# Kernel optimization log

Measured on AMD Instinct MI355X. Metric: run time of the kernel, lower is better.

## Reference

```python
import jax, jax.numpy as jnp
import numpy as np

N_LAYER = 4
N_HEAD = 8
D_HEAD = 64
D_MODEL = 512
D_INNER = 2048
NMT = 16  # num_mem_tokens
BSZ = 1
QLEN = 2048


def _rel_shift(x):
    # x: [i, j, b, n] -> Transformer-XL relative shift
    i, j, b, n = x.shape
    zero_pad = jnp.zeros((i, 1, b, n), dtype=x.dtype)
    x_padded = jnp.concatenate([zero_pad, x], axis=1)  # [i, j+1, b, n]
    x_padded = x_padded.reshape(j + 1, i, b, n)
    return x_padded[1:].reshape(i, j, b, n)


def _layer_norm(x, g, b):
    mu = jnp.mean(x, axis=-1, keepdims=True)
    var = jnp.mean(jnp.square(x - mu), axis=-1, keepdims=True)
    return (x - mu) / jnp.sqrt(var + 1e-5) * g + b


def setup_inputs() -> dict:
    key = jax.random.key(0)
    ks = jax.random.split(key, 12)
    s = 0.02
    return {
        "word_emb": jax.random.normal(ks[0], (BSZ, QLEN, D_MODEL), jnp.float32),
        "mem_tokens": jax.random.normal(ks[1], (NMT, BSZ, D_MODEL), jnp.float32),
        "Wqkv": jax.random.normal(ks[2], (N_LAYER, D_MODEL, 3 * N_HEAD * D_HEAD), jnp.float32) * s,
        "Wr": jax.random.normal(ks[3], (N_LAYER, D_MODEL, N_HEAD * D_HEAD), jnp.float32) * s,
        "Wo": jax.random.normal(ks[4], (N_LAYER, N_HEAD * D_HEAD, D_MODEL), jnp.float32) * s,
        "ln1_scale": jnp.ones((N_LAYER, D_MODEL), jnp.float32),
        "ln1_bias": jnp.zeros((N_LAYER, D_MODEL), jnp.float32),
        "ffn_W1": jax.random.normal(ks[5], (N_LAYER, D_MODEL, D_INNER), jnp.float32) * s,
        "ffn_b1": jnp.zeros((N_LAYER, D_INNER), jnp.float32),
        "ffn_W2": jax.random.normal(ks[6], (N_LAYER, D_INNER, D_MODEL), jnp.float32) * s,
        "ffn_b2": jnp.zeros((N_LAYER, D_MODEL), jnp.float32),
        "ln2_scale": jnp.ones((N_LAYER, D_MODEL), jnp.float32),
        "ln2_bias": jnp.zeros((N_LAYER, D_MODEL), jnp.float32),
        "r_w_bias": jax.random.normal(ks[7], (N_HEAD, D_HEAD), jnp.float32) * s,
        "r_r_bias": jax.random.normal(ks[8], (N_HEAD, D_HEAD), jnp.float32) * s,
    }


def reference(word_emb, mem_tokens, Wqkv, Wr, Wo, ln1_scale, ln1_bias,
              ffn_W1, ffn_b1, ffn_W2, ffn_b2, ln2_scale, ln2_bias,
              r_w_bias, r_r_bias):
    # word_emb: [B, Q, D] -> [Q, B, D]; prepend + append mem tokens (mem_at_end)
    w = jnp.transpose(word_emb, (1, 0, 2))
    w = jnp.concatenate([mem_tokens, w, mem_tokens], axis=0)  # [T, B, D]
    T, B = w.shape[0], w.shape[1]

    # causal mask (mlen=0) with mem-token exceptions, True = masked
    mask = jnp.triu(jnp.ones((T, T), dtype=bool), k=1)
    mask = mask.at[:NMT, :NMT].set(False)          # read-mem block attends to itself
    mask = mask.at[-NMT:, -NMT:].set(False)        # write-mem block attends to itself

    # sinusoidal relative positional embedding, pos_seq = T-1 .. 0
    inv_freq = 1.0 / (10000.0 ** (jnp.arange(0, D_MODEL, 2, dtype=jnp.float32) / D_MODEL))
    pos_seq = jnp.arange(T - 1, -1, -1.0, dtype=jnp.float32)
    sinusoid = pos_seq[:, None] * inv_freq[None, :]
    pos_emb = jnp.concatenate([jnp.sin(sinusoid), jnp.cos(sinusoid)], axis=-1)  # [T, D]

    scale = 1.0 / np.sqrt(D_HEAD)
    for l in range(N_LAYER):
        heads = w @ Wqkv[l]                                        # [T, B, 3*H*Dh]
        q, k, v = jnp.split(heads, 3, axis=-1)
        q = q.reshape(T, B, N_HEAD, D_HEAD)
        k = k.reshape(T, B, N_HEAD, D_HEAD)
        v = v.reshape(T, B, N_HEAD, D_HEAD)
        r = (pos_emb @ Wr[l]).reshape(T, N_HEAD, D_HEAD)           # [T, H, Dh]

        AC = jnp.einsum('ibnd,jbnd->ijbn', q + r_w_bias, k)
        BD = _rel_shift(jnp.einsum('ibnd,jnd->ijbn', q + r_r_bias, r))
        score = (AC + BD) * scale                                  # [T, T, B, H]
        score = jnp.where(mask[:, :, None, None], -1e30, score)
        prob = jax.nn.softmax(score, axis=1)
        attn_vec = jnp.einsum('ijbn,jbnd->ibnd', prob, v).reshape(T, B, N_HEAD * D_HEAD)

        w = _layer_norm(w + attn_vec @ Wo[l], ln1_scale[l], ln1_bias[l])  # post-LN
        ff = jax.nn.relu(w @ ffn_W1[l] + ffn_b1[l]) @ ffn_W2[l] + ffn_b2[l]
        w = _layer_norm(w + ff, ln2_scale[l], ln2_bias[l])
    return w  # [T, B, D]
```

## Files before the change

### kernel.cpp

```cpp
#include <hip/hip_runtime.h>
#include <hip/hip_bf16.h>
#include <math.h>
#include <stdint.h>

#define TT 2080
#define DM 512
#define DI 2048
#define NH 8
#define DH 64
#define NMTOK 16
#define NLAYER 4
#define QKV_N 1536
#define ATT_SCALE 0.125f
#define SPLIT 8
#define WT_STRIDE 3407872
#define QRP_HEAD 2200640

typedef short bf16x8 __attribute__((ext_vector_type(8)));
typedef float f32x4 __attribute__((ext_vector_type(4)));
typedef unsigned short ushort_t;

__device__ __forceinline__ ushort_t f2bf(float f) {
  __hip_bfloat16 h = __float2bfloat16(f);
  return *reinterpret_cast<ushort_t*>(&h);
}
__device__ __forceinline__ float bfbits2f(unsigned int hi_bits) {
  return __uint_as_float(hi_bits);
}
__device__ __forceinline__ float bf2f(ushort_t u) {
  return bfbits2f(((unsigned int)u) << 16);
}
__device__ __forceinline__ void unpack8(uint4 v, float* f) {
  f[0] = bfbits2f(v.x << 16); f[1] = bfbits2f(v.x & 0xffff0000u);
  f[2] = bfbits2f(v.y << 16); f[3] = bfbits2f(v.y & 0xffff0000u);
  f[4] = bfbits2f(v.z << 16); f[5] = bfbits2f(v.z & 0xffff0000u);
  f[6] = bfbits2f(v.w << 16); f[7] = bfbits2f(v.w & 0xffff0000u);
}
__device__ __forceinline__ unsigned int pack2(ushort_t lo, ushort_t hi) {
  return (unsigned int)lo | ((unsigned int)hi << 16);
}
__device__ __forceinline__ void barrier_lds() {
  asm volatile("s_waitcnt lgkmcnt(0)" ::: "memory");
  __builtin_amdgcn_s_barrier();
}
__device__ __forceinline__ void barrier_all() {
  asm volatile("s_waitcnt vmcnt(0) lgkmcnt(0)" ::: "memory");
  __builtin_amdgcn_s_barrier();
}
__device__ __forceinline__ void gload16(const ushort_t* g, ushort_t* l) {
  __builtin_amdgcn_global_load_lds(
      (__attribute__((address_space(1))) void*)(uintptr_t)g,
      (__attribute__((address_space(3))) void*)(uintptr_t)l, 16, 0, 0);
}
__device__ __forceinline__ size_t qr_rowbase(int i) {
  int m = i & 3;
  int r = (m == 0) ? 0 : (m == 1) ? 3 : (m == 2) ? 5 : 6;
  return (size_t)i * (i + 33) / 2 + 6 * (i >> 2) + r;
}
__device__ __forceinline__ size_t ft512(int r, int c) {
  return (((size_t)(r >> 4) * 16 + (c >> 5)) << 9) + (((c >> 3) & 3) << 7) +
         ((r & 15) << 3) + (c & 7);
}

__global__ __launch_bounds__(256) void k_prep(
    const float* __restrict__ Wqkv, const float* __restrict__ Wr,
    const float* __restrict__ Wo, const float* __restrict__ W1,
    const float* __restrict__ W2, ushort_t* __restrict__ dstAll,
    const float* __restrict__ we, const float* __restrict__ mem,
    float* __restrict__ w, ushort_t* __restrict__ wbft,
    ushort_t* __restrict__ posft) {
  const int tid = threadIdx.x;
  if (blockIdx.x >= 13312) {
    int idx = (blockIdx.x - 13312) * 256 + tid;
    if (idx >= TT * DM) return;
    int t = idx >> 9, d = idx & 511;
    float v;
    if (t < NMTOK) v = mem[t * DM + d];
    else if (t < NMTOK + 2048) v = we[(t - NMTOK) * DM + d];
    else v = mem[(t - (NMTOK + 2048)) * DM + d];
    w[idx] = v;
    wbft[ft512(t, d)] = f2bf(v);
    float p = (float)(TT - 1 - t);
    int i2 = d & 255;
    float freq = __expf(-0.035977892f * (float)i2);
    float ang = p * freq;
    posft[ft512(t, d)] = f2bf((d < 256) ? __sinf(ang) : __cosf(ang));
    return;
  }
  __shared__ float tl[32][33];
  const int l = blockIdx.x / 3328;
// ... 165 lines not shown
  const int nIter = (kEnd - kBeg) >> 6;
  stage(smem, kt0);
  __syncthreads();
  for (int t = 0; t < nIter; t += 2) {
    if (t + 1 < nIter) stage(smem + 12288, kt0 + (t + 1) * 2);
    compute(smem);
    __syncthreads();
    if (t + 2 < nIter) stage(smem, kt0 + (t + 2) * 2);
    compute(smem + 12288);
    __syncthreads();
  }

#pragma unroll
  for (int i = 0; i < 2; ++i) {
    const int rowb = m0 + wm + i * 16 + quad * 4;
#pragma unroll
    for (int j = 0; j < 4; ++j) {
      const int col = n0 + wn + j * 16 + lm;
      const float bv = (flags & 1) ? bias[col] : 0.f;
#pragma unroll
      for (int t2 = 0; t2 < 4; ++t2) {
        const int row = rowb + t2;
        float v = acc[i][j][t2] + bv;
        if (flags & 2) v = fmaxf(v, 0.f);
        if (omode == 0) {
          Cf[(size_t)row * N + col] = v;
        } else if (omode == 1) {
          Cb[(size_t)row * N + col] = f2bf(v);
        } else if (omode == 2) {
          Cb[(((size_t)(row >> 4) * cftKT + (col >> 5)) << 9) +
             (((col >> 3) & 3) << 7) + ((row & 15) << 3) + (col & 7)] = f2bf(v);
        } else if (omode == 3) {
          Cb[ft512(row, col)] = f2bf(v + rwb[col]);
          aux[(size_t)row * DM + col] = f2bf(v + rrb[col]);
        } else if (omode == 4) {
          Cb[ft512(row, col - 512)] = f2bf(v);
        } else {
          const int dv = col - 1024;
          Cb[((size_t)(dv >> 4) * 65 + (row >> 5)) * 512 +
             (((row >> 3) & 3) << 7) + ((dv & 15) << 3) + (row & 7)] = f2bf(v);
        }
      }
    }
  }
}

__global__ __launch_bounds__(256) void k_gemm_qkvwr_ft(
    const ushort_t* __restrict__ wbft, const ushort_t* __restrict__ posft,
    const ushort_t* __restrict__ qkvT, const ushort_t* __restrict__ wrT,
    ushort_t* __restrict__ qwft, ushort_t* __restrict__ kft,
    ushort_t* __restrict__ vtft, ushort_t* __restrict__ rbg,
    ushort_t* __restrict__ qrb, const float* __restrict__ rwb,
    const float* __restrict__ rrb) {
  __shared__ ushort_t smem[24576];
  int m0 = blockIdx.y * 64;
  if (m0 + 64 > TT) m0 = TT - 64;
  const int bx = blockIdx.x;
  if (bx < 12) {
    const int om = (bx < 4) ? 3 : (bx < 8 ? 4 : 5);
    ushort_t* dst = (om == 3) ? qwft : (om == 4) ? kft : vtft;
    gemm_ft_body(smem, wbft, qkvT, nullptr, QKV_N, DM, 0, DM, m0, bx * 128,
                 0, om, nullptr, dst, 0, qrb, rwb, rrb);
  } else {
    gemm_ft_body(smem, posft, wrT, nullptr, DM, DM, 0, DM, m0, (bx - 12) * 128,
                 0, 1, nullptr, rbg, 0, nullptr, nullptr, nullptr);
  }
}

__global__ __launch_bounds__(256) void k_ffn1_ft(const ushort_t* __restrict__ wbft,
                                                 const ushort_t* __restrict__ w1T,
                                                 const float* __restrict__ b1l,
                                                 ushort_t* __restrict__ ff1ft) {
  __shared__ ushort_t smem[24576];
  int m0 = blockIdx.y * 64;
  if (m0 + 64 > TT) m0 = TT - 64;
  gemm_ft_body(smem, wbft, w1T, b1l, DI, DM, 0, DM, m0, blockIdx.x * 128,
               1 | 2, 2, nullptr, ff1ft, DI >> 5, nullptr, nullptr, nullptr);
}

__global__ __launch_bounds__(256) void k_ffn2_ft(const ushort_t* __restrict__ ff1ft,
                                                 const ushort_t* __restrict__ w2T,
                                                 const float* __restrict__ b2l,
                                                 float* __restrict__ ff2p) {
  __shared__ ushort_t smem[24576];
  int m0 = blockIdx.y * 64;
  if (m0 + 64 > TT) m0 = TT - 64;
  const int s = blockIdx.z;
  gemm_ft_body(smem, ff1ft, w2T, b2l, DM, DI, s * 512, s * 512 + 512, m0,
               blockIdx.x * 128, (s == 0) ? 1 : 0, 0,
               ff2p + (size_t)s * TT * DM, nullptr, 0, nullptr, nullptr, nullptr);
}

__global__ __launch_bounds__(256) void k_qr(const ushort_t* __restrict__ qrb,
                                            const ushort_t* __restrict__ rbg,
                                            ushort_t* __restrict__ qrp) {
  const int h = blockIdx.z;
  const int m0 = blockIdx.y * 32, n0 = blockIdx.x * 64;
  if (!(n0 == 0 || n0 + 63 >= TT - 32 - m0)) return;
  __shared__ short As[32][72];
  __shared__ short Bs[64][72];
  const int tid = threadIdx.x;
  const int lane = tid & 63, wv = tid >> 6;
  const int wm = (wv >> 1) * 16, wn = (wv & 1) * 32;
  const int lm = lane & 15, quad = lane >> 4;
  const int sr = tid >> 3, sc8 = (tid & 7) * 8;
  const uint4 zero4 = make_uint4(0, 0, 0, 0);

  *(uint4*)&As[sr][sc8] = *(const uint4*)&qrb[(size_t)(m0 + sr) * DM + h * DH + sc8];
  int br0 = n0 + sr, br1 = n0 + sr + 32;
  *(uint4*)&Bs[sr][sc8] =
      (br0 < TT) ? *(const uint4*)&rbg[(size_t)br0 * DM + h * DH + sc8] : zero4;
  *(uint4*)&Bs[sr + 32][sc8] =
      (br1 < TT) ? *(const uint4*)&rbg[(size_t)br1 * DM + h * DH + sc8] : zero4;
  __syncthreads();

  f32x4 acc[2];
  acc[0] = (f32x4)(0.f); acc[1] = (f32x4)(0.f);
#pragma unroll
  for (int kk = 0; kk < 64; kk += 32) {
    bf16x8 a = *(const bf16x8*)&As[wm + lm][kk + quad * 8];
    bf16x8 b0 = *(const bf16x8*)&Bs[wn + lm][kk + quad * 8];
    bf16x8 b1 = *(const bf16x8*)&Bs[wn + 16 + lm][kk + quad * 8];
    acc[0] = __builtin_amdgcn_mfma_f32_16x16x32_bf16(a, b0, acc[0], 0, 0, 0);
    acc[1] = __builtin_amdgcn_mfma_f32_16x16x32_bf16(a, b1, acc[1], 0, 0, 0);
  }
  const size_t hb = (size_t)h * QRP_HEAD;
#pragma unroll
  for (int nt = 0; nt < 2; ++nt) {
    int col = n0 + wn + nt * 16 + lm;
    if (col >= TT) continue;
#pragma unroll
    for (int t = 0; t < 4; ++t) {
      int row = m0 + wm + quad * 4 + t;
      float v = acc[nt][t];
      int p = row + col - (TT - 1);
      size_t rb = hb + qr_rowbase(row);
      if (p >= 0) qrp[rb + p] = f2bf(v);
      if (col < 16) qrp[rb + row + 1 + col] = f2bf(v);
    }
  }
}

__global__ __launch_bounds__(256) void k_attn(const ushort_t* __restrict__ qwft,
                                              const ushort_t* __restrict__ kft,
                                              const ushort_t* __restrict__ vtft,
                                              const ushort_t* __restrict__ qrp,
                                              float* __restrict__ mlP,
                                              ushort_t* __restrict__ opP) {
  const int h = blockIdx.y;
  const int qt = 64 - blockIdx.x;
  const int c = blockIdx.z;
  if (c > qt) return;
  const int i0 = qt * 32;
  const int tid = threadIdx.x;
  const int lane = tid & 63, wv = tid >> 6;
  const int lm = lane & 15, quad = lane >> 4;

  __shared__ ushort_t qwl[2048];
  __shared__ ushort_t kl[2][2048];
  __shared__ ushort_t vtl[2][2048];
  __shared__ ushort_t pbl[1024];
  __shared__ float st[32][34];
  __shared__ float m_s[32], l_s[32], alpha_s[32];

  const int ii = tid >> 3, g = tid & 7, jjb = g * 4;
  const int i = i0 + ii;
  const size_t hb = (size_t)h * QRP_HEAD;
  const size_t qrRow = hb + qr_rowbase(i);
  const size_t qrRowW = hb + qr_rowbase(i + 1) + i + 2;

  const int sblk = tid >> 6, sln = tid & 63;
  auto stageKV = [&](int j0, int buf) {
    gload16(kft + (((size_t)((j0 >> 4) + (sblk >> 1)) * 16) + h * 2 + (sblk & 1)) * 512 +
                (sln << 3),
            kl[buf] + (tid << 3));
    gload16(vtft + (((size_t)(h * 4 + sblk)) * 65 + (j0 >> 5)) * 512 + (sln << 3),
            vtl[buf] + (tid << 3));
  };

  gload16(qwft + (((size_t)((i0 >> 4) + (sblk >> 1)) * 16) + h * 2 + (sblk & 1)) * 512 +
              (sln << 3),
          qwl + (tid << 3));
  stageKV(c * 32, 0);
  if (tid < 32) { m_s[tid] = -INFINITY; l_s[tid] = 0.f; }
  barrier_all();

  const int acit = wv >> 1, acjt = wv & 1;
  bf16x8 aQ[2];
#pragma unroll
  for (int kt = 0; kt < 2; ++kt)
    aQ[kt] = *(const bf16x8*)&qwl[(acit * 2 + kt) * 512 + (lane << 3)];

  f32x4 oA = (f32x4)(0.f);
  f32x4 oB = (f32x4)(0.f);

  int cur = 0;
  for (int jt = c; jt <= qt; jt += SPLIT) {
    const int j0 = jt * 32;
    uint2 qr2 = *(const uint2*)&qrp[qrRow + j0 + jjb];
    if (jt + SPLIT <= qt) stageKV((jt + SPLIT) * 32, cur ^ 1);

    {
      f32x4 ac = (f32x4)(0.f);
#pragma unroll
      for (int kt = 0; kt < 2; ++kt) {
        bf16x8 b = *(const bf16x8*)&kl[cur][(acjt * 2 + kt) * 512 + (lane << 3)];
        ac = __builtin_amdgcn_mfma_f32_16x16x32_bf16(aQ[kt], b, ac, 0, 0, 0);
      }
#pragma unroll
      for (int t = 0; t < 4; ++t)
        st[acit * 16 + quad * 4 + t][acjt * 16 + lm] = ac[t];
    }
    barrier_lds();

    {
      float bd4[4];
      bd4[0] = bf2f((ushort_t)(qr2.x & 0xffffu));
      bd4[1] = bf2f((ushort_t)(qr2.x >> 16));
      bd4[2] = bf2f((ushort_t)(qr2.y & 0xffffu));
      bd4[3] = bf2f((ushort_t)(qr2.y >> 16));
      float sreg[4];
      if (jt < qt) {
#pragma unroll
        for (int u = 0; u < 4; ++u)
          sreg[u] = (st[ii][jjb + u] + bd4[u]) * ATT_SCALE;
      } else {
#pragma unroll
        for (int u = 0; u < 4; ++u) {
          int j = j0 + jjb + u;
          float acv = st[ii][jjb + u];
          float s;
          if (j <= i) {
            s = (acv + bd4[u]) * ATT_SCALE;
          } else {
            bool inmem = (i < NMTOK && j < NMTOK) ||
                         (i >= TT - NMTOK && j >= TT - NMTOK);
            if (!inmem) s = -1e30f;
            else if (j == i + 1) s = acv * ATT_SCALE;
            else s = (acv + bf2f(qrp[qrRowW + (j - i - 2)])) * ATT_SCALE;
          }
          sreg[u] = s;
        }
      }
      float tmax = fmaxf(fmaxf(sreg[0], sreg[1]), fmaxf(sreg[2], sreg[3]));
#pragma unroll
      for (int off = 1; off < 8; off <<= 1) tmax = fmaxf(tmax, __shfl_xor(tmax, off));
      const float mold = m_s[ii];
      const float mnew = fmaxf(mold, tmax);
      const float alpha = __expf(mold - mnew);
      float p[4], psum = 0.f;
#pragma unroll
      for (int u = 0; u < 4; ++u) { p[u] = __expf(sreg[u] - mnew); psum += p[u]; }
#pragma unroll
      for (int off = 1; off < 8; off <<= 1) psum += __shfl_xor(psum, off);
      uint2 pk;
      pk.x = pack2(f2bf(p[0]), f2bf(p[1]));
      pk.y = pack2(f2bf(p[2]), f2bf(p[3]));
      *(uint2*)&pbl[(size_t)(ii >> 4) * 512 + (g >> 1) * 128 + (ii & 15) * 8 +
                    (g & 1) * 4] = pk;
      if (g == 0) {
        m_s[ii] = mnew;
        l_s[ii] = l_s[ii] * alpha + psum;
        alpha_s[ii] = alpha;
      }
    }
    barrier_lds();

    {
      float a0 = alpha_s[lm], a1 = alpha_s[16 + lm];
      bf16x8 av = *(const bf16x8*)&vtl[cur][wv * 512 + (lane << 3)];
      bf16x8 p0 = *(const bf16x8*)&pbl[(lane << 3)];
      bf16x8 p1 = *(const bf16x8*)&pbl[512 + (lane << 3)];
#pragma unroll
      for (int t = 0; t < 4; ++t) { oA[t] *= a0; oB[t] *= a1; }
      oA = __builtin_amdgcn_mfma_f32_16x16x32_bf16(av, p0, oA, 0, 0, 0);
      oB = __builtin_amdgcn_mfma_f32_16x16x32_bf16(av, p1, oB, 0, 0, 0);
    }
    barrier_all();
    cur ^= 1;
  }

  {
    const int pidx = (qt * NH + h) * SPLIT + c;
    if (tid < 32) {
      mlP[(size_t)pidx * 64 + tid] = m_s[tid];
      mlP[(size_t)pidx * 64 + 32 + tid] = l_s[tid];
    }
    ushort_t o0[4], o1[4];
#pragma unroll
    for (int t = 0; t < 4; ++t) { o0[t] = f2bf(oA[t]); o1[t] = f2bf(oB[t]); }
    size_t ob = (size_t)pidx * 2048;
    *(uint2*)&opP[ob + (size_t)lm * 64 + wv * 16 + quad * 4] = *(uint2*)o0;
    *(uint2*)&opP[ob + (size_t)(16 + lm) * 64 + wv * 16 + quad * 4] = *(uint2*)o1;
  }
}

__global__ __launch_bounds__(256) void k_attn_combine(const float* __restrict__ mlP,
                                                      const ushort_t* __restrict__ opP,
                                                      ushort_t* __restrict__ attnb) {
  const int qt = blockIdx.x, h = blockIdx.y;
  const int nc = (qt + 1 < SPLIT) ? qt + 1 : SPLIT;
  const int tid = threadIdx.x;
  const int i = tid >> 3, d8 = (tid & 7) * 8;
  const size_t base = (size_t)(qt * NH + h) * SPLIT;
  float m[SPLIT], l[SPLIT], wgt[SPLIT];
  float M = -INFINITY;
  for (int cc = 0; cc < nc; ++cc) {
    m[cc] = mlP[(base + cc) * 64 + i];
    l[cc] = mlP[(base + cc) * 64 + 32 + i];
    M = fmaxf(M, m[cc]);
  }
  float L = 0.f;
  for (int cc = 0; cc < nc; ++cc) { wgt[cc] = __expf(m[cc] - M); L += l[cc] * wgt[cc]; }
  float acc[8] = {0, 0, 0, 0, 0, 0, 0, 0};
  for (int cc = 0; cc < nc; ++cc) {
    uint4 v = *(const uint4*)&opP[(base + cc) * 2048 + (size_t)i * 64 + d8];
    float f[8]; unpack8(v, f);
#pragma unroll
    for (int k = 0; k < 8; ++k) acc[k] += wgt[cc] * f[k];
  }
  const float inv = 1.f / L;
  ushort_t o8[8];
#pragma unroll
  for (int k = 0; k < 8; ++k) o8[k] = f2bf(acc[k] * inv);
  *(uint4*)&attnb[(size_t)(qt * 32 + i) * DM + h * DH + d8] = *(uint4*)o8;
}

__global__ __launch_bounds__(256) void k_addln(const float* __restrict__ w,
                                               float* __restrict__ wout,
                                               ushort_t* __restrict__ wbft,
                                               const float* __restrict__ delta,
                                               int nparts,
                                               const float* __restrict__ gamma,
                                               const float* __restrict__ beta) {
  const int row = blockIdx.x;
  const int tid = threadIdx.x;
  __shared__ float red[4], red2[4];
  __shared__ float sm[512];
// ... 31 lines not shown
    for (int e = 0; e < 8; ++e) t8[e] = f2bf(sm[d8 + e]);
    *(uint4*)&wbft[ft512(row, d8)] = *(uint4*)t8;
  }
}

extern "C" void kernel_launch(void* const* d_in, const int* in_sizes, int n_in,
                              void* d_out, int out_size, void* d_ws, size_t ws_size,
                              hipStream_t stream) {
  const float* we   = (const float*)d_in[0];
  const float* mem  = (const float*)d_in[1];
  const float* Wqkv = (const float*)d_in[2];
  const float* Wr   = (const float*)d_in[3];
  const float* Wo   = (const float*)d_in[4];
  const float* ln1s = (const float*)d_in[5];
  const float* ln1b = (const float*)d_in[6];
  const float* W1   = (const float*)d_in[7];
  const float* b1   = (const float*)d_in[8];
  const float* W2   = (const float*)d_in[9];
  const float* b2   = (const float*)d_in[10];
  const float* ln2s = (const float*)d_in[11];
  const float* ln2b = (const float*)d_in[12];
  const float* rwb  = (const float*)d_in[13];
  const float* rrb  = (const float*)d_in[14];

  float* w     = (float*)d_ws;
  float* proj  = w + (size_t)TT * DM;
  ushort_t* wbft  = (ushort_t*)(proj + (size_t)TT * DM);
  ushort_t* posft = wbft + (size_t)TT * DM;
  ushort_t* attnb = posft + (size_t)TT * DM;
  ushort_t* qkvB  = attnb + (size_t)TT * DM;
  ushort_t* qwft  = qkvB;
  ushort_t* kft   = qkvB + (size_t)TT * DM;
  ushort_t* vtft  = qkvB + (size_t)2 * TT * DM;
  ushort_t* rbg   = qkvB + (size_t)TT * QKV_N;
  ushort_t* WtAll = rbg + (size_t)TT * DM;
  ushort_t* opP   = WtAll + (size_t)NLAYER * WT_STRIDE;
  float* mlP   = (float*)(opP + (size_t)65 * 8 * SPLIT * 2048);
  ushort_t* qrb  = (ushort_t*)(mlP + (size_t)65 * 8 * SPLIT * 64);
  ushort_t* qrp  = qrb + (size_t)TT * DM;
  ushort_t* ff1ft = qkvB;
  float* ff2p  = (float*)opP;
  const size_t OFF_QKVT = 0, OFF_WRT = 786432, OFF_WOT = 1048576,
               OFF_W1T = 1310720, OFF_W2T = 2359296;

  k_prep<<<13312 + 4160, 256, 0, stream>>>(Wqkv, Wr, Wo, W1, W2, WtAll,
                                           we, mem, w, wbft, posft);

  dim3 gQW(16, 33);
  dim3 gW1(16, 33);
  dim3 gW2(4, 33, 4);
  dim3 gDM32(DM / 64, 65);
  dim3 gQR(33, 65, NH);
  dim3 gA(65, NH, SPLIT);
  dim3 gC(65, NH);

  for (int l = 0; l < NLAYER; ++l) {
    const ushort_t* Wt = WtAll + (size_t)l * WT_STRIDE;
    k_gemm_qkvwr_ft<<<gQW, 256, 0, stream>>>(wbft, posft, Wt + OFF_QKVT,
                                             Wt + OFF_WRT, qwft, kft, vtft,
                                             rbg, qrb, rwb, rrb);
    k_qr<<<gQR, 256, 0, stream>>>(qrb, rbg, qrp);
    k_attn<<<gA, 256, 0, stream>>>(qwft, kft, vtft, qrp, mlP, opP);
    k_attn_combine<<<gC, 256, 0, stream>>>(mlP, opP, attnb);
    k_gemm_mfma<<<gDM32, 256, 0, stream>>>(attnb, Wt + OFF_WOT, nullptr, proj, nullptr,
                                           DM, DM, 0);
    k_addln<<<TT, 256, 0, stream>>>(w, w, wbft, proj, 1,
                                    ln1s + (size_t)l * DM, ln1b + (size_t)l * DM);
    k_ffn1_ft<<<gW1, 256, 0, stream>>>(wbft, Wt + OFF_W1T, b1 + (size_t)l * DI, ff1ft);
    k_ffn2_ft<<<gW2, 256, 0, stream>>>(ff1ft, Wt + OFF_W2T, b2 + (size_t)l * DM, ff2p);
    float* wout = (l == NLAYER - 1) ? (float*)d_out : w;
    k_addln<<<TT, 256, 0, stream>>>(w, wout, wbft, ff2p, 4,
                                    ln2s + (size_t)l * DM, ln2b + (size_t)l * DM);
  }
}
```

Before: 610.7 us.

## Restructure attention to per-wave register flash tiles with fragment-ordered BD layout

Each wave in the attention kernel now processes its own strided set of 32-column key tiles for a 32-row query tile. Q, K, V fragments and the partial softmax state are held in registers instead of block-shared LDS staging with block-wide barriers, and only a per-wave LDS scratch is used to re-layout P. The k_qr kernel now writes the relative-position term in a tile-blocked layout that matches the MFMA output fragments, and stores the wrap-around values in a separate small buffer that reuses the attnb space. The grid drops the split dimension, with 4 wave-chunks per block feeding the combine step. This trades block-level synchronisation and LDS double-buffering for more register pressure, direct global loads with no reuse across waves, and fewer blocks in flight.

```diff
diff --git a/kernel.cpp b/kernel.cpp
--- a/kernel.cpp
+++ b/kernel.cpp
@@ -12,9 +12,10 @@
 #define NLAYER 4
 #define QKV_N 1536
 #define ATT_SCALE 0.125f
-#define SPLIT 8
+#define NCH 4
 #define WT_STRIDE 3407872
-#define QRP_HEAD 2200640
+#define BDF_HEAD 2196480
+#define WRAP_HEAD 33280
 
 typedef short bf16x8 __attribute__((ext_vector_type(8)));
 typedef float f32x4 __attribute__((ext_vector_type(4)));
@@ -43,19 +44,10 @@
   asm volatile("s_waitcnt lgkmcnt(0)" ::: "memory");
   __builtin_amdgcn_s_barrier();
 }
-__device__ __forceinline__ void barrier_all() {
-  asm volatile("s_waitcnt vmcnt(0) lgkmcnt(0)" ::: "memory");
-  __builtin_amdgcn_s_barrier();
-}
 __device__ __forceinline__ void gload16(const ushort_t* g, ushort_t* l) {
   __builtin_amdgcn_global_load_lds(
       (__attribute__((address_space(1))) void*)(uintptr_t)g,
       (__attribute__((address_space(3))) void*)(uintptr_t)l, 16, 0, 0);
-}
-__device__ __forceinline__ size_t qr_rowbase(int i) {
-  int m = i & 3;
-  int r = (m == 0) ? 0 : (m == 1) ? 3 : (m == 2) ? 5 : 6;
-  return (size_t)i * (i + 33) / 2 + 6 * (i >> 2) + r;
 }
 __device__ __forceinline__ size_t ft512(int r, int c) {
   return (((size_t)(r >> 4) * 16 + (c >> 5)) << 9) + (((c >> 3) & 3) << 7) +
@@ -348,7 +340,8 @@
 
 __global__ __launch_bounds__(256) void k_qr(const ushort_t* __restrict__ qrb,
                                             const ushort_t* __restrict__ rbg,
-                                            ushort_t* __restrict__ qrp) {
+                                            ushort_t* __restrict__ bdf,
+                                            ushort_t* __restrict__ wrapv) {
   const int h = blockIdx.z;
   const int m0 = blockIdx.y * 32, n0 = blockIdx.x * 64;
   if (!(n0 == 0 || n0 + 63 >= TT - 32 - m0)) return;
@@ -379,7 +372,8 @@
     acc[0] = __builtin_amdgcn_mfma_f32_16x16x32_bf16(a, b0, acc[0], 0, 0, 0);
     acc[1] = __builtin_amdgcn_mfma_f32_16x16x32_bf16(a, b1, acc[1], 0, 0, 0);
   }
-  const size_t hb = (size_t)h * QRP_HEAD;
+  const size_t hb = (size_t)h * BDF_HEAD;
+  const size_t hw = (size_t)h * WRAP_HEAD;
 #pragma unroll
   for (int nt = 0; nt < 2; ++nt) {
     int col = n0 + wn + nt * 16 + lm;
@@ -388,10 +382,17 @@
     for (int t = 0; t < 4; ++t) {
       int row = m0 + wm + quad * 4 + t;
       float v = acc[nt][t];
+      ushort_t vb = f2bf(v);
       int p = row + col - (TT - 1);
-      size_t rb = hb + qr_rowbase(row);
-      if (p >= 0) qrp[rb + p] = f2bf(v);
-      if (col < 16) qrp[rb + row + 1 + col] = f2bf(v);
+      if (p >= 0) {
+        int qti = row >> 5, jti = p >> 5;
+        int ri = row & 31, cj = p & 31;
+        size_t tb = hb + (((size_t)(qti * (qti + 1) / 2 + jti)) << 10);
+        size_t off = (size_t)((((ri >> 4) * 2 + (cj >> 4)) << 8) +
+                              ((((ri & 15) >> 2) * 16 + (cj & 15)) << 2) + (ri & 3));
+        bdf[tb + off] = vb;
+      }
+      if (col < 16) wrapv[hw + row * 16 + col] = vb;
     }
   }
 }
@@ -399,166 +400,240 @@
 __global__ __launch_bounds__(256) void k_attn(const ushort_t* __restrict__ qwft,
                                               const ushort_t* __restrict__ kft,
                                               const ushort_t* __restrict__ vtft,
-                                              const ushort_t* __restrict__ qrp,
+                                              const ushort_t* __restrict__ bdf,
+                                              const ushort_t* __restrict__ wrapv,
                                               float* __restrict__ mlP,
                                               ushort_t* __restrict__ opP) {
   const int h = blockIdx.y;
   const int qt = 64 - blockIdx.x;
-  const int c = blockIdx.z;
-  if (c > qt) return;
+  const int tid = threadIdx.x;
+  const int wv = tid >> 6;
+  if (wv > qt) return;
+  const int lane = tid & 63;
+  const int lm = lane & 15, quad = lane >> 4;
   const int i0 = qt * 32;
-  const int tid = threadIdx.x;
-  const int lane = tid & 63, wv = tid >> 6;
-  const int lm = lane & 15, quad = lane >> 4;
-
-  __shared__ ushort_t qwl[2048];
-  __shared__ ushort_t kl[2][2048];
-  __shared__ ushort_t vtl[2][2048];
-  __shared__ ushort_t pbl[1024];
-  __shared__ float st[32][34];
-  __shared__ float m_s[32], l_s[32], alpha_s[32];
-
-  const int ii = tid >> 3, g = tid & 7, jjb = g * 4;
-  const int i = i0 + ii;
-  const size_t hb = (size_t)h * QRP_HEAD;
-  const size_t qrRow = hb + qr_rowbase(i);
-  const size_t qrRowW = hb + qr_rowbase(i + 1) + i + 2;
-
-  const int sblk = tid >> 6, sln = tid & 63;
-  auto stageKV = [&](int j0, int buf) {
-    gload16(kft + (((size_t)((j0 >> 4) + (sblk >> 1)) * 16) + h * 2 + (sblk & 1)) * 512 +
-                (sln << 3),
-            kl[buf] + (tid << 3));
-    gload16(vtft + (((size_t)(h * 4 + sblk)) * 65 + (j0 >> 5)) * 512 + (sln << 3),
-            vtl[buf] + (tid << 3));
-  };
-
-  gload16(qwft + (((size_t)((i0 >> 4) + (sblk >> 1)) * 16) + h * 2 + (sblk & 1)) * 512 +
-              (sln << 3),
-          qwl + (tid << 3));
-  stageKV(c * 32, 0);
-  if (tid < 32) { m_s[tid] = -INFINITY; l_s[tid] = 0.f; }
-  barrier_all();
-
-  const int acit = wv >> 1, acjt = wv & 1;
-  bf16x8 aQ[2];
-#pragma unroll
-  for (int kt = 0; kt < 2; ++kt)
-    aQ[kt] = *(const bf16x8*)&qwl[(acit * 2 + kt) * 512 + (lane << 3)];
-
-  f32x4 oA = (f32x4)(0.f);
-  f32x4 oB = (f32x4)(0.f);
-
-  int cur = 0;
-  for (int jt = c; jt <= qt; jt += SPLIT) {
+
+  __shared__ ushort_t pbl[4][1024];
+
+  bf16x8 qf[2][2];
+#pragma unroll
+  for (int qi = 0; qi < 2; ++qi)
+#pragma unroll
+    for (int kt = 0; kt < 2; ++kt)
+      qf[qi][kt] = *(const bf16x8*)&qwft[(((size_t)((i0 >> 4) + qi) * 16) +
+                                         h * 2 + kt) * 512 + (lane << 3)];
+
+  const size_t hbd = (size_t)h * BDF_HEAD + (((size_t)(qt * (qt + 1) / 2)) << 10);
+  const size_t hwr = (size_t)h * WRAP_HEAD;
+
+  float mreg[2][4], lreg[2][4];
+#pragma unroll
+  for (int qi = 0; qi < 2; ++qi)
+#pragma unroll
+    for (int t = 0; t < 4; ++t) { mreg[qi][t] = -INFINITY; lreg[qi][t] = 0.f; }
+  f32x4 o[4][2];
+#pragma unroll
+  for (int dt = 0; dt < 4; ++dt)
+#pragma unroll
+    for (int iq = 0; iq < 2; ++iq) o[dt][iq] = (f32x4)(0.f);
+
+  for (int jt = wv; jt <= qt; jt += NCH) {
     const int j0 = jt * 32;
-    uint2 qr2 = *(const uint2*)&qrp[qrRow + j0 + jjb];
-    if (jt + SPLIT <= qt) stageKV((jt + SPLIT) * 32, cur ^ 1);
-
+    bf16x8 kf[2][2];
+#pragma unroll
+    for (int jq = 0; jq < 2; ++jq)
+#pragma unroll
+      for (int kt = 0; kt < 2; ++kt)
+        kf[jq][kt] = *(const bf16x8*)&kft[(((size_t)((j0 >> 4) + jq) * 16) +
+                                          h * 2 + kt) * 512 + (lane << 3)];
+    bf16x8 vf[4];
+#pragma unroll
+    for (int dt = 0; dt < 4; ++dt)
+      vf[dt] = *(const bf16x8*)&vtft[(((size_t)(h * 4 + dt)) * 65 + jt) * 512 +
+                                     (lane << 3)];
+    uint2 bd[2][2];
+#pragma unroll
+    for (int qi = 0; qi < 2; ++qi)
+#pragma unroll
+      for (int jq = 0; jq < 2; ++jq)
+        bd[qi][jq] = *(const uint2*)&bdf[hbd + ((size_t)jt << 10) +
+                                         ((qi * 2 + jq) << 8) + (lane << 2)];
+
+    f32x4 sA[2][2];
+#pragma unroll
+    for (int qi = 0; qi < 2; ++qi)
+#pragma unroll
+      for (int jq = 0; jq < 2; ++jq) {
+        f32x4 ac = (f32x4)(0.f);
+#pragma unroll
+        for (int kt = 0; kt < 2; ++kt)
+          ac = __builtin_amdgcn_mfma_f32_16x16x32_bf16(qf[qi][kt], kf[jq][kt], ac, 0, 0, 0);
+        sA[qi][jq] = ac;
+      }
+
+    if (jt < qt) {
+#pragma unroll
+      for (int qi = 0; qi < 2; ++qi)
+#pragma unroll
+        for (int jq = 0; jq < 2; ++jq) {
+          float b0 = bf2f((ushort_t)(bd[qi][jq].x & 0xffffu));
+          float b1 = bf2f((ushort_t)(bd[qi][jq].x >> 16));
+          float b2 = bf2f((ushort_t)(bd[qi][jq].y & 0xffffu));
+          float b3 = bf2f((ushort_t)(bd[qi][jq].y >> 16));
+          sA[qi][jq][0] = (sA[qi][jq][0] + b0) * ATT_SCALE;
+          sA[qi][jq][1] = (sA[qi][jq][1] + b1) * ATT_SCALE;
+          sA[qi][jq][2] = (sA[qi][jq][2] + b2) * ATT_SCALE;
+          sA[qi][jq][3] = (sA[qi][jq][3] + b3) * ATT_SCALE;
+        }
+    } else {
+#pragma unroll
+      for (int qi = 0; qi < 2; ++qi)
+#pragma unroll
+        for (int jq = 0; jq < 2; ++jq) {
+          float bdv[4];
+          bdv[0] = bf2f((ushort_t)(bd[qi][jq].x & 0xffffu));
+          bdv[1] = bf2f((ushort_t)(bd[qi][jq].x >> 16));
+          bdv[2] = bf2f((ushort_t)(bd[qi][jq].y & 0xffffu));
+          bdv[3] = bf2f((ushort_t)(bd[qi][jq].y >> 16));
+          const int j = j0 + jq * 16 + lm;
+#pragma unroll
+          for (int t = 0; t < 4; ++t) {
+            const int i = i0 + qi * 16 + quad * 4 + t;
+            const float acv = sA[qi][jq][t];
+            float s;
+            if (j <= i) {
+              s = (acv + bdv[t]) * ATT_SCALE;
+            } else {
+              bool inmem = (i < NMTOK && j < NMTOK) ||
+                           (i >= TT - NMTOK && j >= TT - NMTOK);
+              if (!inmem) s = -1e30f;
+              else if (j == i + 1) s = acv * ATT_SCALE;
+              else s = (acv + bf2f(wrapv[hwr + (i + 1) * 16 + (j - i - 2)])) * ATT_SCALE;
+            }
+            sA[qi][jq][t] = s;
+          }
+        }
+    }
+
+    float mx[2][4];
+#pragma unroll
+    for (int qi = 0; qi < 2; ++qi)
+#pragma unroll
+      for (int t = 0; t < 4; ++t)
+        mx[qi][t] = fmaxf(sA[qi][0][t], sA[qi][1][t]);
+#pragma unroll
+    for (int off = 1; off < 16; off <<= 1)
+#pragma unroll
+      for (int qi = 0; qi < 2; ++qi)
+#pragma unroll
+        for (int t = 0; t < 4; ++t)
+          mx[qi][t] = fmaxf(mx[qi][t], __shfl_xor(mx[qi][t], off));
+    float al[2][4];
+#pragma unroll
+    for (int qi = 0; qi < 2; ++qi)
+#pragma unroll
+      for (int t = 0; t < 4; ++t) {
+        float mnew = fmaxf(mreg[qi][t], mx[qi][t]);
+        al[qi][t] = __expf(mreg[qi][t] - mnew);
+        mreg[qi][t] = mnew;
+      }
+    float ps[2][4];
+#pragma unroll
+    for (int qi = 0; qi < 2; ++qi)
+#pragma unroll
+      for (int t = 0; t < 4; ++t) {
+        sA[qi][0][t] = __expf(sA[qi][0][t] - mreg[qi][t]);
+        sA[qi][1][t] = __expf(sA[qi][1][t] - mreg[qi][t]);
+        ps[qi][t] = sA[qi][0][t] + sA[qi][1][t];
+      }
+#pragma unroll
+    for (int off = 1; off < 16; off <<= 1)
+#pragma unroll
+      for (int qi = 0; qi < 2; ++qi)
+#pragma unroll
+        for (int t = 0; t < 4; ++t)
+          ps[qi][t] += __shfl_xor(ps[qi][t], off);
+#pragma unroll
+    for (int qi = 0; qi < 2; ++qi)
+#pragma unroll
+      for (int t = 0; t < 4; ++t)
+        lreg[qi][t] = lreg[qi][t] * al[qi][t] + ps[qi][t];
+
+    float aw[2];
     {
-      f32x4 ac = (f32x4)(0.f);
-#pragma unroll
-      for (int kt = 0; kt < 2; ++kt) {
-        bf16x8 b = *(const bf16x8*)&kl[cur][(acjt * 2 + kt) * 512 + (lane << 3)];
-        ac = __builtin_amdgcn_mfma_f32_16x16x32_bf16(aQ[kt], b, ac, 0, 0, 0);
+      const int src = (lm >> 2) << 4;
+      const int t3 = lm & 3;
+#pragma unroll
+      for (int iq = 0; iq < 2; ++iq) {
+        float g0 = __shfl(al[iq][0], src);
+        float g1 = __shfl(al[iq][1], src);
+        float g2 = __shfl(al[iq][2], src);
+        float g3 = __shfl(al[iq][3], src);
+        aw[iq] = (t3 == 0) ? g0 : (t3 == 1) ? g1 : (t3 == 2) ? g2 : g3;
       }
-#pragma unroll
-      for (int t = 0; t < 4; ++t)
-        st[acit * 16 + quad * 4 + t][acjt * 16 + lm] = ac[t];
-    }
-    barrier_lds();
-
-    {
-      float bd4[4];
-      bd4[0] = bf2f((ushort_t)(qr2.x & 0xffffu));
-      bd4[1] = bf2f((ushort_t)(qr2.x >> 16));
-      bd4[2] = bf2f((ushort_t)(qr2.y & 0xffffu));
-      bd4[3] = bf2f((ushort_t)(qr2.y >> 16));
-      float sreg[4];
-      if (jt < qt) {
-#pragma unroll
-        for (int u = 0; u < 4; ++u)
-          sreg[u] = (st[ii][jjb + u] + bd4[u]) * ATT_SCALE;
-      } else {
-#pragma unroll
-        for (int u = 0; u < 4; ++u) {
-          int j = j0 + jjb + u;
-          float acv = st[ii][jjb + u];
-          float s;
-          if (j <= i) {
-            s = (acv + bd4[u]) * ATT_SCALE;
-          } else {
-            bool inmem = (i < NMTOK && j < NMTOK) ||
-                         (i >= TT - NMTOK && j >= TT - NMTOK);
-            if (!inmem) s = -1e30f;
-            else if (j == i + 1) s = acv * ATT_SCALE;
-            else s = (acv + bf2f(qrp[qrRowW + (j - i - 2)])) * ATT_SCALE;
-          }
-          sreg[u] = s;
-        }
+    }
+#pragma unroll
+    for (int dt = 0; dt < 4; ++dt)
+#pragma unroll
+      for (int iq = 0; iq < 2; ++iq)
+#pragma unroll
+        for (int tt = 0; tt < 4; ++tt) o[dt][iq][tt] *= aw[iq];
+
+#pragma unroll
+    for (int qi = 0; qi < 2; ++qi)
+#pragma unroll
+      for (int jq = 0; jq < 2; ++jq)
+#pragma unroll
+        for (int t = 0; t < 4; ++t)
+          pbl[wv][(qi << 9) +
+                  (((jq * 2 + (lm >> 3)) * 16 + (quad * 4 + t)) << 3) +
+                  (lm & 7)] = f2bf(sA[qi][jq][t]);
+    asm volatile("s_waitcnt lgkmcnt(0)" ::: "memory");
+    __builtin_amdgcn_sched_barrier(0);
+    bf16x8 pf[2];
+#pragma unroll
+    for (int iq = 0; iq < 2; ++iq)
+      pf[iq] = *(const bf16x8*)&pbl[wv][(iq << 9) + (lane << 3)];
+
+#pragma unroll
+    for (int dt = 0; dt < 4; ++dt)
+#pragma unroll
+      for (int iq = 0; iq < 2; ++iq)
+        o[dt][iq] = __builtin_amdgcn_mfma_f32_16x16x32_bf16(vf[dt], pf[iq], o[dt][iq], 0, 0, 0);
+  }
+
+  const int pidx = (qt * NH + h) * NCH + wv;
+  if (lm == 0) {
+#pragma unroll
+    for (int qi = 0; qi < 2; ++qi)
+#pragma unroll
+      for (int t = 0; t < 4; ++t) {
+        mlP[(size_t)pidx * 64 + qi * 16 + quad * 4 + t] = mreg[qi][t];
+        mlP[(size_t)pidx * 64 + 32 + qi * 16 + quad * 4 + t] = lreg[qi][t];
       }
-      float tmax = fmaxf(fmaxf(sreg[0], sreg[1]), fmaxf(sreg[2], sreg[3]));
-#pragma unroll
-      for (int off = 1; off < 8; off <<= 1) tmax = fmaxf(tmax, __shfl_xor(tmax, off));
-      const float mold = m_s[ii];
-      const float mnew = fmaxf(mold, tmax);
-      const float alpha = __expf(mold - mnew);
-      float p[4], psum = 0.f;
-#pragma unroll
-      for (int u = 0; u < 4; ++u) { p[u] = __expf(sreg[u] - mnew); psum += p[u]; }
-#pragma unroll
-      for (int off = 1; off < 8; off <<= 1) psum += __shfl_xor(psum, off);
-      uint2 pk;
-      pk.x = pack2(f2bf(p[0]), f2bf(p[1]));
-      pk.y = pack2(f2bf(p[2]), f2bf(p[3]));
-      *(uint2*)&pbl[(size_t)(ii >> 4) * 512 + (g >> 1) * 128 + (ii & 15) * 8 +
-                    (g & 1) * 4] = pk;
-      if (g == 0) {
-        m_s[ii] = mnew;
-        l_s[ii] = l_s[ii] * alpha + psum;
-        alpha_s[ii] = alpha;
-      }
-    }
-    barrier_lds();
-
-    {
-      float a0 = alpha_s[lm], a1 = alpha_s[16 + lm];
-      bf16x8 av = *(const bf16x8*)&vtl[cur][wv * 512 + (lane << 3)];
-      bf16x8 p0 = *(const bf16x8*)&pbl[(lane << 3)];
-      bf16x8 p1 = *(const bf16x8*)&pbl[512 + (lane << 3)];
-#pragma unroll
-      for (int t = 0; t < 4; ++t) { oA[t] *= a0; oB[t] *= a1; }
-      oA = __builtin_amdgcn_mfma_f32_16x16x32_bf16(av, p0, oA, 0, 0, 0);
-      oB = __builtin_amdgcn_mfma_f32_16x16x32_bf16(av, p1, oB, 0, 0, 0);
-    }
-    barrier_all();
-    cur ^= 1;
-  }
-
-  {
-    const int pidx = (qt * NH + h) * SPLIT + c;
-    if (tid < 32) {
-      mlP[(size_t)pidx * 64 + tid] = m_s[tid];
-      mlP[(size_t)pidx * 64 + 32 + tid] = l_s[tid];
-    }
-    ushort_t o0[4], o1[4];
-#pragma unroll
-    for (int t = 0; t < 4; ++t) { o0[t] = f2bf(oA[t]); o1[t] = f2bf(oB[t]); }
-    size_t ob = (size_t)pidx * 2048;
-    *(uint2*)&opP[ob + (size_t)lm * 64 + wv * 16 + quad * 4] = *(uint2*)o0;
-    *(uint2*)&opP[ob + (size_t)(16 + lm) * 64 + wv * 16 + quad * 4] = *(uint2*)o1;
-  }
+  }
+  const size_t ob = (size_t)pidx * 2048;
+#pragma unroll
+  for (int iq = 0; iq < 2; ++iq)
+#pragma unroll
+    for (int dt = 0; dt < 4; ++dt) {
+      ushort_t o4[4];
+#pragma unroll
+      for (int tt = 0; tt < 4; ++tt) o4[tt] = f2bf(o[dt][iq][tt]);
+      *(uint2*)&opP[ob + (size_t)(iq * 16 + lm) * 64 + dt * 16 + quad * 4] =
+          *(uint2*)o4;
+    }
 }
 
 __global__ __launch_bounds__(256) void k_attn_combine(const float* __restrict__ mlP,
                                                       const ushort_t* __restrict__ opP,
                                                       ushort_t* __restrict__ attnb) {
   const int qt = blockIdx.x, h = blockIdx.y;
-  const int nc = (qt + 1 < SPLIT) ? qt + 1 : SPLIT;
+  const int nc = (qt + 1 < NCH) ? qt + 1 : NCH;
   const int tid = threadIdx.x;
   const int i = tid >> 3, d8 = (tid & 7) * 8;
-  const size_t base = (size_t)(qt * NH + h) * SPLIT;
-  float m[SPLIT], l[SPLIT], wgt[SPLIT];
+  const size_t base = (size_t)(qt * NH + h) * NCH;
+  float m[NCH], l[NCH], wgt[NCH];
   float M = -INFINITY;
   for (int cc = 0; cc < nc; ++cc) {
     m[cc] = mlP[(base + cc) * 64 + i];
@@ -659,9 +734,10 @@
   ushort_t* rbg   = qkvB + (size_t)TT * QKV_N;
   ushort_t* WtAll = rbg + (size_t)TT * DM;
   ushort_t* opP   = WtAll + (size_t)NLAYER * WT_STRIDE;
-  float* mlP   = (float*)(opP + (size_t)65 * 8 * SPLIT * 2048);
-  ushort_t* qrb  = (ushort_t*)(mlP + (size_t)65 * 8 * SPLIT * 64);
-  ushort_t* qrp  = qrb + (size_t)TT * DM;
+  float* mlP   = (float*)(opP + (size_t)65 * 8 * 8 * 2048);
+  ushort_t* qrb  = (ushort_t*)(mlP + (size_t)65 * 8 * 8 * 64);
+  ushort_t* bdf  = qrb + (size_t)TT * DM;
+  ushort_t* wrapv = attnb;
   ushort_t* ff1ft = qkvB;
   float* ff2p  = (float*)opP;
   const size_t OFF_QKVT = 0, OFF_WRT = 786432, OFF_WOT = 1048576,
@@ -675,7 +751,7 @@
   dim3 gW2(4, 33, 4);
   dim3 gDM32(DM / 64, 65);
   dim3 gQR(33, 65, NH);
-  dim3 gA(65, NH, SPLIT);
+  dim3 gA(65, NH);
   dim3 gC(65, NH);
 
   for (int l = 0; l < NLAYER; ++l) {
@@ -683,8 +759,8 @@
     k_gemm_qkvwr_ft<<<gQW, 256, 0, stream>>>(wbft, posft, Wt + OFF_QKVT,
                                              Wt + OFF_WRT, qwft, kft, vtft,
                                              rbg, qrb, rwb, rrb);
-    k_qr<<<gQR, 256, 0, stream>>>(qrb, rbg, qrp);
-    k_attn<<<gA, 256, 0, stream>>>(qwft, kft, vtft, qrp, mlP, opP);
+    k_qr<<<gQR, 256, 0, stream>>>(qrb, rbg, bdf, wrapv);
+    k_attn<<<gA, 256, 0, stream>>>(qwft, kft, vtft, bdf, wrapv, mlP, opP);
     k_attn_combine<<<gC, 256, 0, stream>>>(mlP, opP, attnb);
     k_gemm_mfma<<<gDM32, 256, 0, stream>>>(attnb, Wt + OFF_WOT, nullptr, proj, nullptr,
                                            DM, DM, 0);
```

Result: slower. 676.2 us (+10.7%).

## Fuse relative-position BD term into attention kernel via shuffled MFMA

Applied to the files above, without the earlier changes.

Removes the separate k_qr kernel that precomputed the shifted BD scores into a packed global buffer. The attention kernel now computes Q·R tiles with extra MFMAs and applies the relative shift through lane shuffles, reading R in a fragment-tiled layout stored at a one-row offset. A small k_wrap kernel covers the 16 wrap-around memory-token entries. This drops a large global write/read of BD scores per layer, at the cost of extra MFMAs, shuffles and R loads inside the attention loop.

```diff
diff --git a/kernel.cpp b/kernel.cpp
--- a/kernel.cpp
+++ b/kernel.cpp
@@ -14,7 +14,7 @@
 #define ATT_SCALE 0.125f
 #define SPLIT 8
 #define WT_STRIDE 3407872
-#define QRP_HEAD 2200640
+#define RSFT_ROWS 2112
 
 typedef short bf16x8 __attribute__((ext_vector_type(8)));
 typedef float f32x4 __attribute__((ext_vector_type(4)));
@@ -51,11 +51,6 @@
   __builtin_amdgcn_global_load_lds(
       (__attribute__((address_space(1))) void*)(uintptr_t)g,
       (__attribute__((address_space(3))) void*)(uintptr_t)l, 16, 0, 0);
-}
-__device__ __forceinline__ size_t qr_rowbase(int i) {
-  int m = i & 3;
-  int r = (m == 0) ? 0 : (m == 1) ? 3 : (m == 2) ? 5 : 6;
-  return (size_t)i * (i + 33) / 2 + 6 * (i >> 2) + r;
 }
 __device__ __forceinline__ size_t ft512(int r, int c) {
   return (((size_t)(r >> 4) * 16 + (c >> 5)) << 9) + (((c >> 3) & 3) << 7) +
@@ -287,13 +282,16 @@
              (((col >> 3) & 3) << 7) + ((row & 15) << 3) + (col & 7)] = f2bf(v);
         } else if (omode == 3) {
           Cb[ft512(row, col)] = f2bf(v + rwb[col]);
-          aux[(size_t)row * DM + col] = f2bf(v + rrb[col]);
+          aux[ft512(row, col)] = f2bf(v + rrb[col]);
         } else if (omode == 4) {
           Cb[ft512(row, col - 512)] = f2bf(v);
-        } else {
+        } else if (omode == 5) {
           const int dv = col - 1024;
           Cb[((size_t)(dv >> 4) * 65 + (row >> 5)) * 512 +
              (((row >> 3) & 3) << 7) + ((dv & 15) << 3) + (row & 7)] = f2bf(v);
+        } else {
+          Cb[ft512(row + 1, col)] = f2bf(v);
+          if (row < 16) aux[(size_t)row * 512 + col] = f2bf(v);
         }
       }
     }
@@ -304,9 +302,9 @@
     const ushort_t* __restrict__ wbft, const ushort_t* __restrict__ posft,
     const ushort_t* __restrict__ qkvT, const ushort_t* __restrict__ wrT,
     ushort_t* __restrict__ qwft, ushort_t* __restrict__ kft,
-    ushort_t* __restrict__ vtft, ushort_t* __restrict__ rbg,
-    ushort_t* __restrict__ qrb, const float* __restrict__ rwb,
-    const float* __restrict__ rrb) {
+    ushort_t* __restrict__ vtft, ushort_t* __restrict__ rsft,
+    ushort_t* __restrict__ r16, ushort_t* __restrict__ qrft,
+    const float* __restrict__ rwb, const float* __restrict__ rrb) {
   __shared__ ushort_t smem[24576];
   int m0 = blockIdx.y * 64;
   if (m0 + 64 > TT) m0 = TT - 64;
@@ -315,10 +313,10 @@
     const int om = (bx < 4) ? 3 : (bx < 8 ? 4 : 5);
     ushort_t* dst = (om == 3) ? qwft : (om == 4) ? kft : vtft;
     gemm_ft_body(smem, wbft, qkvT, nullptr, QKV_N, DM, 0, DM, m0, bx * 128,
-                 0, om, nullptr, dst, 0, qrb, rwb, rrb);
+                 0, om, nullptr, dst, 0, (om == 3) ? qrft : nullptr, rwb, rrb);
   } else {
     gemm_ft_body(smem, posft, wrT, nullptr, DM, DM, 0, DM, m0, (bx - 12) * 128,
-                 0, 1, nullptr, rbg, 0, nullptr, nullptr, nullptr);
+                 0, 6, nullptr, rsft, 0, r16, nullptr, nullptr);
   }
 }
 
@@ -346,60 +344,36 @@
                ff2p + (size_t)s * TT * DM, nullptr, 0, nullptr, nullptr, nullptr);
 }
 
-__global__ __launch_bounds__(256) void k_qr(const ushort_t* __restrict__ qrb,
-                                            const ushort_t* __restrict__ rbg,
-                                            ushort_t* __restrict__ qrp) {
-  const int h = blockIdx.z;
-  const int m0 = blockIdx.y * 32, n0 = blockIdx.x * 64;
-  if (!(n0 == 0 || n0 + 63 >= TT - 32 - m0)) return;
-  __shared__ short As[32][72];
-  __shared__ short Bs[64][72];
-  const int tid = threadIdx.x;
-  const int lane = tid & 63, wv = tid >> 6;
-  const int wm = (wv >> 1) * 16, wn = (wv & 1) * 32;
-  const int lm = lane & 15, quad = lane >> 4;
-  const int sr = tid >> 3, sc8 = (tid & 7) * 8;
-  const uint4 zero4 = make_uint4(0, 0, 0, 0);
-
-  *(uint4*)&As[sr][sc8] = *(const uint4*)&qrb[(size_t)(m0 + sr) * DM + h * DH + sc8];
-  int br0 = n0 + sr, br1 = n0 + sr + 32;
-  *(uint4*)&Bs[sr][sc8] =
-      (br0 < TT) ? *(const uint4*)&rbg[(size_t)br0 * DM + h * DH + sc8] : zero4;
-  *(uint4*)&Bs[sr + 32][sc8] =
-      (br1 < TT) ? *(const uint4*)&rbg[(size_t)br1 * DM + h * DH + sc8] : zero4;
-  __syncthreads();
-
-  f32x4 acc[2];
-  acc[0] = (f32x4)(0.f); acc[1] = (f32x4)(0.f);
-#pragma unroll
-  for (int kk = 0; kk < 64; kk += 32) {
-    bf16x8 a = *(const bf16x8*)&As[wm + lm][kk + quad * 8];
-    bf16x8 b0 = *(const bf16x8*)&Bs[wn + lm][kk + quad * 8];
-    bf16x8 b1 = *(const bf16x8*)&Bs[wn + 16 + lm][kk + quad * 8];
-    acc[0] = __builtin_amdgcn_mfma_f32_16x16x32_bf16(a, b0, acc[0], 0, 0, 0);
-    acc[1] = __builtin_amdgcn_mfma_f32_16x16x32_bf16(a, b1, acc[1], 0, 0, 0);
-  }
-  const size_t hb = (size_t)h * QRP_HEAD;
-#pragma unroll
-  for (int nt = 0; nt < 2; ++nt) {
-    int col = n0 + wn + nt * 16 + lm;
-    if (col >= TT) continue;
-#pragma unroll
-    for (int t = 0; t < 4; ++t) {
-      int row = m0 + wm + quad * 4 + t;
-      float v = acc[nt][t];
-      int p = row + col - (TT - 1);
-      size_t rb = hb + qr_rowbase(row);
-      if (p >= 0) qrp[rb + p] = f2bf(v);
-      if (col < 16) qrp[rb + row + 1 + col] = f2bf(v);
-    }
-  }
+__global__ __launch_bounds__(256) void k_wrap(const ushort_t* __restrict__ qrft,
+                                              const ushort_t* __restrict__ r16,
+                                              ushort_t* __restrict__ wrapv) {
+  const int h = blockIdx.y;
+  const int row = blockIdx.x * 32 + (threadIdx.x >> 3);
+  const int w = threadIdx.x & 7;
+  float a0 = 0.f, a1 = 0.f;
+#pragma unroll
+  for (int d8 = 0; d8 < 64; d8 += 8) {
+    bf16x8 qv = *(const bf16x8*)&qrft[ft512(row, h * DH + d8)];
+    bf16x8 r0 = *(const bf16x8*)&r16[(size_t)w * 512 + h * DH + d8];
+    bf16x8 r1 = *(const bf16x8*)&r16[(size_t)(w + 8) * 512 + h * DH + d8];
+#pragma unroll
+    for (int e = 0; e < 8; ++e) {
+      float q = bf2f((ushort_t)qv[e]);
+      a0 += q * bf2f((ushort_t)r0[e]);
+      a1 += q * bf2f((ushort_t)r1[e]);
+    }
+  }
+  const size_t b = (size_t)h * TT * 16 + (size_t)row * 16;
+  wrapv[b + w] = f2bf(a0);
+  wrapv[b + w + 8] = f2bf(a1);
 }
 
 __global__ __launch_bounds__(256) void k_attn(const ushort_t* __restrict__ qwft,
+                                              const ushort_t* __restrict__ qrft,
                                               const ushort_t* __restrict__ kft,
                                               const ushort_t* __restrict__ vtft,
-                                              const ushort_t* __restrict__ qrp,
+                                              const ushort_t* __restrict__ rsft,
+                                              const ushort_t* __restrict__ wrapv,
                                               float* __restrict__ mlP,
                                               ushort_t* __restrict__ opP) {
   const int h = blockIdx.y;
@@ -420,9 +394,7 @@
 
   const int ii = tid >> 3, g = tid & 7, jjb = g * 4;
   const int i = i0 + ii;
-  const size_t hb = (size_t)h * QRP_HEAD;
-  const size_t qrRow = hb + qr_rowbase(i);
-  const size_t qrRowW = hb + qr_rowbase(i + 1) + i + 2;
+  const size_t hwr = (size_t)h * TT * 16;
 
   const int sblk = tid >> 6, sln = tid & 63;
   auto stageKV = [&](int j0, int buf) {
@@ -433,18 +405,34 @@
             vtl[buf] + (tid << 3));
   };
 
+  const int acit = wv >> 1, acjt = wv & 1;
+  const int cqlo = 1 + acjt - acit;
+  auto loadRS = [&](int jt2, bf16x8 (&rs)[2][2]) {
+    const int wbp4 = 128 - 2 * (qt - jt2);
+#pragma unroll
+    for (int f = 0; f < 2; ++f)
+#pragma unroll
+      for (int kt = 0; kt < 2; ++kt)
+        rs[f][kt] = *(const bf16x8*)&rsft[(((size_t)(wbp4 + cqlo + f) * 16) +
+                                          h * 2 + kt) * 512 + (lane << 3)];
+  };
+
   gload16(qwft + (((size_t)((i0 >> 4) + (sblk >> 1)) * 16) + h * 2 + (sblk & 1)) * 512 +
               (sln << 3),
           qwl + (tid << 3));
   stageKV(c * 32, 0);
+  bf16x8 rsc[2][2];
+  loadRS(c, rsc);
   if (tid < 32) { m_s[tid] = -INFINITY; l_s[tid] = 0.f; }
   barrier_all();
 
-  const int acit = wv >> 1, acjt = wv & 1;
-  bf16x8 aQ[2];
-#pragma unroll
-  for (int kt = 0; kt < 2; ++kt)
+  bf16x8 aQ[2], aQR[2];
+#pragma unroll
+  for (int kt = 0; kt < 2; ++kt) {
     aQ[kt] = *(const bf16x8*)&qwl[(acit * 2 + kt) * 512 + (lane << 3)];
+    aQR[kt] = *(const bf16x8*)&qrft[(((size_t)((i0 >> 4) + acit) * 16) +
+                                    h * 2 + kt) * 512 + (lane << 3)];
+  }
 
   f32x4 oA = (f32x4)(0.f);
   f32x4 oB = (f32x4)(0.f);
@@ -452,47 +440,55 @@
   int cur = 0;
   for (int jt = c; jt <= qt; jt += SPLIT) {
     const int j0 = jt * 32;
-    uint2 qr2 = *(const uint2*)&qrp[qrRow + j0 + jjb];
     if (jt + SPLIT <= qt) stageKV((jt + SPLIT) * 32, cur ^ 1);
+    const int jn = (jt + SPLIT <= qt) ? jt + SPLIT : jt;
+    bf16x8 rsn[2][2];
+    loadRS(jn, rsn);
 
     {
-      f32x4 ac = (f32x4)(0.f);
+      f32x4 ac = (f32x4)(0.f), qa = (f32x4)(0.f), qb = (f32x4)(0.f);
 #pragma unroll
       for (int kt = 0; kt < 2; ++kt) {
         bf16x8 b = *(const bf16x8*)&kl[cur][(acjt * 2 + kt) * 512 + (lane << 3)];
         ac = __builtin_amdgcn_mfma_f32_16x16x32_bf16(aQ[kt], b, ac, 0, 0, 0);
+        qa = __builtin_amdgcn_mfma_f32_16x16x32_bf16(aQR[kt], rsc[0][kt], qa, 0, 0, 0);
+        qb = __builtin_amdgcn_mfma_f32_16x16x32_bf16(aQR[kt], rsc[1][kt], qb, 0, 0, 0);
       }
-#pragma unroll
-      for (int t = 0; t < 4; ++t)
-        st[acit * 16 + quad * 4 + t][acjt * 16 + lm] = ac[t];
+      const bool diag = (jt == qt);
+      const int thr = 16 * (1 + acit - acjt);
+#pragma unroll
+      for (int t = 0; t < 4; ++t) {
+        const int idx = lm - (quad * 4 + t) + 16;
+        const int src = quad * 16 + (idx & 15);
+        const float av = __shfl(qa[t], src);
+        const float bv2 = __shfl(qb[t], src);
+        float bd = (idx < 16) ? av : bv2;
+        if (diag && idx > thr) bd = 0.f;
+        st[acit * 16 + quad * 4 + t][acjt * 16 + lm] = ac[t] + bd;
+      }
     }
     barrier_lds();
 
     {
-      float bd4[4];
-      bd4[0] = bf2f((ushort_t)(qr2.x & 0xffffu));
-      bd4[1] = bf2f((ushort_t)(qr2.x >> 16));
-      bd4[2] = bf2f((ushort_t)(qr2.y & 0xffffu));
-      bd4[3] = bf2f((ushort_t)(qr2.y >> 16));
       float sreg[4];
       if (jt < qt) {
 #pragma unroll
-        for (int u = 0; u < 4; ++u)
-          sreg[u] = (st[ii][jjb + u] + bd4[u]) * ATT_SCALE;
+        for (int u = 0; u < 4; ++u) sreg[u] = st[ii][jjb + u] * ATT_SCALE;
       } else {
 #pragma unroll
         for (int u = 0; u < 4; ++u) {
           int j = j0 + jjb + u;
-          float acv = st[ii][jjb + u];
+          float stv = st[ii][jjb + u];
           float s;
           if (j <= i) {
-            s = (acv + bd4[u]) * ATT_SCALE;
+            s = stv * ATT_SCALE;
           } else {
             bool inmem = (i < NMTOK && j < NMTOK) ||
                          (i >= TT - NMTOK && j >= TT - NMTOK);
             if (!inmem) s = -1e30f;
-            else if (j == i + 1) s = acv * ATT_SCALE;
-            else s = (acv + bf2f(qrp[qrRowW + (j - i - 2)])) * ATT_SCALE;
+            else if (j == i + 1) s = stv * ATT_SCALE;
+            else s = (stv + bf2f(wrapv[hwr + (size_t)(i + 1) * 16 + (j - i - 2)])) *
+                     ATT_SCALE;
           }
           sreg[u] = s;
         }
@@ -533,6 +529,10 @@
     }
     barrier_all();
     cur ^= 1;
+#pragma unroll
+    for (int f = 0; f < 2; ++f)
+#pragma unroll
+      for (int kt = 0; kt < 2; ++kt) rsc[f][kt] = rsn[f][kt];
   }
 
   {
@@ -656,12 +656,13 @@
   ushort_t* qwft  = qkvB;
   ushort_t* kft   = qkvB + (size_t)TT * DM;
   ushort_t* vtft  = qkvB + (size_t)2 * TT * DM;
-  ushort_t* rbg   = qkvB + (size_t)TT * QKV_N;
-  ushort_t* WtAll = rbg + (size_t)TT * DM;
+  ushort_t* WtAll = qkvB + (size_t)TT * QKV_N + (size_t)TT * DM;
   ushort_t* opP   = WtAll + (size_t)NLAYER * WT_STRIDE;
   float* mlP   = (float*)(opP + (size_t)65 * 8 * SPLIT * 2048);
-  ushort_t* qrb  = (ushort_t*)(mlP + (size_t)65 * 8 * SPLIT * 64);
-  ushort_t* qrp  = qrb + (size_t)TT * DM;
+  ushort_t* qrft  = (ushort_t*)(mlP + (size_t)65 * 8 * SPLIT * 64);
+  ushort_t* rsft  = qrft + (size_t)TT * DM;
+  ushort_t* wrapv = rsft + (size_t)(RSFT_ROWS / 16) * 16 * 512;
+  ushort_t* r16   = wrapv + (size_t)NH * TT * 16;
   ushort_t* ff1ft = qkvB;
   float* ff2p  = (float*)opP;
   const size_t OFF_QKVT = 0, OFF_WRT = 786432, OFF_WOT = 1048576,
@@ -674,7 +675,7 @@
   dim3 gW1(16, 33);
   dim3 gW2(4, 33, 4);
   dim3 gDM32(DM / 64, 65);
-  dim3 gQR(33, 65, NH);
+  dim3 gWr(65, NH);
   dim3 gA(65, NH, SPLIT);
   dim3 gC(65, NH);
 
@@ -682,9 +683,9 @@
     const ushort_t* Wt = WtAll + (size_t)l * WT_STRIDE;
     k_gemm_qkvwr_ft<<<gQW, 256, 0, stream>>>(wbft, posft, Wt + OFF_QKVT,
                                              Wt + OFF_WRT, qwft, kft, vtft,
-                                             rbg, qrb, rwb, rrb);
-    k_qr<<<gQR, 256, 0, stream>>>(qrb, rbg, qrp);
-    k_attn<<<gA, 256, 0, stream>>>(qwft, kft, vtft, qrp, mlP, opP);
+                                             rsft, r16, qrft, rwb, rrb);
+    k_wrap<<<gWr, 256, 0, stream>>>(qrft, r16, wrapv);
+    k_attn<<<gA, 256, 0, stream>>>(qwft, qrft, kft, vtft, rsft, wrapv, mlP, opP);
     k_attn_combine<<<gC, 256, 0, stream>>>(mlP, opP, attnb);
     k_gemm_mfma<<<gDM32, 256, 0, stream>>>(attnb, Wt + OFF_WOT, nullptr, proj, nullptr,
                                            DM, DM, 0);
```

Result: no change. 607.0 us (-0.6%).
